# Performance work log

Measured on AMD Instinct MI355X. Metric: run time of the kernel, lower is better.

Reference implementation:

```python
import jax, jax.numpy as jnp
import numpy as np

EMBED_DIM = 2048
NUM_HEADS = 16
HEAD_DIM = EMBED_DIM // NUM_HEADS
LATENT_DIM = 512


def setup_inputs() -> dict:
    key = jax.random.key(0)
    ks = jax.random.split(key, 6)
    s = 1.0 / np.sqrt(EMBED_DIM)
    sl = 1.0 / np.sqrt(LATENT_DIM)
    x = jax.random.normal(ks[0], (2, 2048, EMBED_DIM), dtype=jnp.float32)
    # nn.Linear stores weight as [out, in]; we keep [in, out] for x @ W
    W_q = jax.random.uniform(ks[1], (EMBED_DIM, EMBED_DIM), jnp.float32, -s, s)
    W_c = jax.random.uniform(ks[2], (EMBED_DIM, LATENT_DIM), jnp.float32, -s, s)
    W_k = jax.random.uniform(ks[3], (LATENT_DIM, EMBED_DIM), jnp.float32, -sl, sl)
    W_v = jax.random.uniform(ks[4], (LATENT_DIM, EMBED_DIM), jnp.float32, -sl, sl)
    W_o = jax.random.uniform(ks[5], (EMBED_DIM, EMBED_DIM), jnp.float32, -s, s)
    return {"x": x, "W_q": W_q, "W_c": W_c, "W_k": W_k, "W_v": W_v, "W_o": W_o}


def reference(x, W_q, W_c, W_k, W_v, W_o):
    B, S, _ = x.shape
    H, D = NUM_HEADS, HEAD_DIM
    Q = (x @ W_q).reshape(B, S, H, D)          # [B,S,H,D]
    C = x @ W_c                                 # [B,S,latent]
    K = (C @ W_k).reshape(B, S, H, D)
    V = (C @ W_v).reshape(B, S, H, D)
    scale = 1.0 / np.sqrt(D).astype(np.float32)
    scores = jnp.einsum('bqhd,bkhd->bhqk', Q, K) * scale
    probs = jax.nn.softmax(scores, axis=-1)
    attn = jnp.einsum('bhqk,bkhd->bqhd', probs, V).reshape(B, S, H * D)
    return attn @ W_o
```

## Files before the change

### kernel.cpp

```cpp
#include <hip/hip_runtime.h>
#include <hip/hip_bf16.h>
#include <cstdint>
#include <cstddef>

#define EDIM 2048
#define SLEN 2048
#define BATCH 2
#define NH 16
#define HD 128
#define LAT 512
#define MROWS (BATCH * SLEN)

#define QPREMUL (0.08838834764831845f * 1.44269504088896340f)

typedef __bf16 bf16;
typedef __bf16 bf16x8 __attribute__((ext_vector_type(8)));
typedef __bf16 bf16x4 __attribute__((ext_vector_type(4)));
typedef float f32x4 __attribute__((ext_vector_type(4)));
typedef float f32x16 __attribute__((ext_vector_type(16)));

#define AS1 __attribute__((address_space(1)))
#define AS3 __attribute__((address_space(3)))

__device__ __forceinline__ void gload_lds16(const void* g, void* l) {
  __builtin_amdgcn_global_load_lds((const AS1 void*)g, (AS3 void*)l, 16, 0, 0);
}

__global__ __launch_bounds__(256) void cvt_f32_bf16(const float* __restrict__ in,
                                                    bf16* __restrict__ out, int n4) {
  int i = blockIdx.x * blockDim.x + threadIdx.x;
  int stride = gridDim.x * blockDim.x;
  for (; i < n4; i += stride) {
    float4 v = reinterpret_cast<const float4*>(in)[i];
    bf16x4 o = {(bf16)v.x, (bf16)v.y, (bf16)v.z, (bf16)v.w};
    reinterpret_cast<bf16x4*>(out)[i] = o;
  }
}

__global__ __launch_bounds__(256) void transpose_cvt(const float* __restrict__ W,
                                                     bf16* __restrict__ Wt,
                                                     int K, int N) {
  __shared__ float tile[32][33];
  const int tx = threadIdx.x, ty = threadIdx.y;
  const int n0 = blockIdx.x * 32, k0 = blockIdx.y * 32;
#pragma unroll
  for (int i = 0; i < 4; ++i)
    tile[ty + i * 8][tx] = W[(size_t)(k0 + ty + i * 8) * N + n0 + tx];
  __syncthreads();
#pragma unroll
  for (int i = 0; i < 4; ++i)
    Wt[(size_t)(n0 + ty + i * 8) * K + k0 + tx] = (bf16)tile[tx][ty + i * 8];
}

enum { P_F32 = 0, P_QC = 1, P_FRAGKV = 2 };

#define BUFSZ 24576

#define STAGE_B_UNIT(dstbuf, k0)                                                 \
  {                                                                              \
    _Pragma("unroll") for (int jj = 0; jj < 2; ++jj) {                           \
      int L = t + jj * 512;                                                      \
      int row = L >> 3, c = L & 7;                                               \
      gload_lds16(Bt + (size_t)(n0 + row) * K + (k0) + ((c ^ (row & 7)) << 3),   \
                  (dstbuf) + 16384 + L * 8);                                     \
    }                                                                            \
  }

#define STAGE_A_PART(dstbuf, k0, jj)                                             \
  {                                                                              \
    int L = t256 + (jj) * 256;                                                   \
    int row = ahalf * 128 + (L >> 3), c = L & 7;                                 \
    gload_lds16(A + (size_t)(m0 + row) * K + (k0) + ((c ^ (row & 7)) << 3),      \
                (dstbuf) + row * 64 + c * 8);                                    \
  }

template <int MODE>
__global__ __launch_bounds__(512, 1)
void gemm8p(const bf16* __restrict__ A, const bf16* __restrict__ Bt,
            float* __restrict__ Cf, bf16* __restrict__ Cb, bf16* __restrict__ Cb2,
            int M, int N, int K) {
  extern __shared__ bf16 lds[];
  const int t = threadIdx.x;
  const int wid = t >> 6, l = t & 63, lo = l & 15, hi = l >> 4;
  const int wr = wid >> 1, wc = wid & 1;
  const int lin = blockIdx.y * gridDim.x + blockIdx.x;
  const int cpx = (gridDim.x * gridDim.y) >> 3;
  const int sw = (lin & 7) * cpx + (lin >> 3);
  const int m0 = (sw / gridDim.x) * 256, n0 = (sw % gridDim.x) * 128;
  const int nk = K >> 6;
  const int t256 = t & 255, ahalf = t >> 8;

  int aoff[2][4], boff[2][4];
#pragma unroll
  for (int kk = 0; kk < 2; ++kk)
#pragma unroll
    for (int m = 0; m < 4; ++m) {
      int ra = wr * 64 + m * 16 + lo;
      aoff[kk][m] = ra * 64 + (((kk * 4 + hi) ^ (ra & 7)) << 3);
      int rb = wc * 64 + m * 16 + lo;
      boff[kk][m] = 16384 + rb * 64 + (((kk * 4 + hi) ^ (rb & 7)) << 3);
    }

  f32x4 acc[4][4] = {};

  {
    bf16* b0 = lds;
    STAGE_B_UNIT(b0, 0);
    STAGE_A_PART(b0, 0, 0); STAGE_A_PART(b0, 0, 1);
    STAGE_A_PART(b0, 0, 2); STAGE_A_PART(b0, 0, 3);
    if (nk > 1) {
      bf16* b1 = lds + BUFSZ;
      STAGE_B_UNIT(b1, 64);
      STAGE_A_PART(b1, 64, 0); STAGE_A_PART(b1, 64, 1);
      STAGE_A_PART(b1, 64, 2); STAGE_A_PART(b1, 64, 3);
      asm volatile("s_waitcnt vmcnt(6)" ::: "memory");
    } else {
      asm volatile("s_waitcnt vmcnt(0)" ::: "memory");
    }
    __builtin_amdgcn_s_barrier();
  }

  int bsel = 0;
  for (int tt = 0; tt < nk; ++tt) {
    bf16* buf = lds + bsel * BUFSZ;
    bf16* nb = lds + ((bsel + 2) % 3) * BUFSZ;
    const bool pre = (tt + 2) < nk;
    const int k2 = (tt + 2) << 6;
    bf16x8 af[4], bfr[4];

#pragma unroll
    for (int m = 0; m < 4; ++m) af[m] = *reinterpret_cast<const bf16x8*>(buf + aoff[0][m]);
#pragma unroll
    for (int n = 0; n < 4; ++n) bfr[n] = *reinterpret_cast<const bf16x8*>(buf + boff[0][n]);
    if (pre) {
      STAGE_B_UNIT(nb, k2);
      STAGE_A_PART(nb, k2, 0); STAGE_A_PART(nb, k2, 1);
    }
    __builtin_amdgcn_s_barrier();
    asm volatile("s_waitcnt lgkmcnt(0)" ::: "memory");
    __builtin_amdgcn_s_setprio(1);
#pragma unroll
    for (int m = 0; m < 4; ++m)
#pragma unroll
      for (int n = 0; n < 4; ++n)
        acc[m][n] = __builtin_amdgcn_mfma_f32_16x16x32_bf16(af[m], bfr[n], acc[m][n], 0, 0, 0);
    __builtin_amdgcn_s_setprio(0);
    __builtin_amdgcn_s_barrier();

#pragma unroll
    for (int m = 0; m < 4; ++m) af[m] = *reinterpret_cast<const bf16x8*>(buf + aoff[1][m]);
#pragma unroll
    for (int n = 0; n < 4; ++n) bfr[n] = *reinterpret_cast<const bf16x8*>(buf + boff[1][n]);
    if (pre) { STAGE_A_PART(nb, k2, 2); STAGE_A_PART(nb, k2, 3); }
    __builtin_amdgcn_s_barrier();
    asm volatile("s_waitcnt lgkmcnt(0)" ::: "memory");
    __builtin_amdgcn_s_setprio(1);
#pragma unroll
    for (int m = 0; m < 4; ++m)
#pragma unroll
      for (int n = 0; n < 4; ++n)
        acc[m][n] = __builtin_amdgcn_mfma_f32_16x16x32_bf16(af[m], bfr[n], acc[m][n], 0, 0, 0);
    __builtin_amdgcn_s_setprio(0);
    if (tt < nk - 2) {
      asm volatile("s_waitcnt vmcnt(6)" ::: "memory");
    } else if (tt == nk - 2) {
      asm volatile("s_waitcnt vmcnt(0)" ::: "memory");
    }
    __builtin_amdgcn_s_barrier();
    bsel = (bsel == 2) ? 0 : bsel + 1;
  }

  const int bb = m0 >> 11, m0r = m0 & 2047;

  if constexpr (MODE == P_F32) {
#pragma unroll
    for (int m = 0; m < 4; ++m) {
      const int rowb = m0 + wr * 64 + m * 16 + hi * 4;
#pragma unroll
      for (int n = 0; n < 4; ++n) {
        const int col = n0 + wc * 64 + n * 16 + lo;
        f32x4 v = acc[m][n];
#pragma unroll
        for (int r = 0; r < 4; ++r) Cf[(size_t)(rowb + r) * N + col] = v[r];
      }
    }
  } else if (MODE == P_QC && n0 >= EDIM) {
#pragma unroll
    for (int m = 0; m < 4; ++m) {
      const int rowb = m0 + wr * 64 + m * 16 + hi * 4;
#pragma unroll
      for (int n = 0; n < 4; ++n) {
        const int col = n0 + wc * 64 + n * 16 + lo;
        f32x4 v = acc[m][n];
#pragma unroll
        for (int r = 0; r < 4; ++r)
          Cb2[(size_t)(rowb + r) * LAT + (col - EDIM)] = (bf16)v[r];
      }
    }
  } else if (MODE == P_FRAGKV && n0 >= EDIM) {
    __syncthreads();
#pragma unroll
    for (int m = 0; m < 4; ++m) {
      const int row0 = wr * 64 + m * 16 + hi * 4;
#pragma unroll
      for (int n = 0; n < 4; ++n) {
        const int colr = wc * 64 + n * 16 + lo;
        f32x4 v = acc[m][n];
        bf16x4 pk = {(bf16)v[0], (bf16)v[1], (bf16)v[2], (bf16)v[3]};
        *reinterpret_cast<bf16x4*>(lds + colr * 264 + row0) = pk;
      }
    }
    __syncthreads();
    const int hv = (n0 - EDIM) >> 7;
#pragma unroll
    for (int k2i = 0; k2i < 8; ++k2i) {
      int c = t + k2i * 512;
      int qs64 = c >> 10, d7b = (c >> 8) & 3, sb = (c >> 5) & 7, d7l = c & 31;
      int col = d7b * 32 + d7l, row = qs64 * 64 + sb * 8;
      bf16x8 val = *reinterpret_cast<const bf16x8*>(lds + col * 264 + row);
      size_t addr = (((size_t)(bb * NH + hv) * 32 + (m0r >> 6) + qs64) << 14) + 8192 +
                    d7b * 2048 + sb * 256 + d7l * 8;
      *reinterpret_cast<bf16x8*>(Cb + addr) = val;
    }
  } else {
    constexpr bool ISQ = (MODE == P_QC);
    __syncthreads();
#pragma unroll
    for (int m = 0; m < 4; ++m) {
      const int row0 = wr * 64 + m * 16 + hi * 4;
#pragma unroll
      for (int n = 0; n < 4; ++n) {
        const int colr = wc * 64 + n * 16 + lo;
        f32x4 v = acc[m][n];
#pragma unroll
        for (int r = 0; r < 4; ++r)
          lds[(row0 + r) * 132 + colr] = ISQ ? (bf16)(v[r] * QPREMUL) : (bf16)v[r];
      }
    }
    __syncthreads();
    const int hh = n0 >> 7;
#pragma unroll
    for (int k2i = 0; k2i < 8; ++k2i) {
      int c = t + k2i * 512;
      int qsub = c >> 9, frag = (c >> 5) & 15, lane = c & 31;
      int row = qsub * 32 + lane;
      bf16x4 lo4 = *reinterpret_cast<const bf16x4*>(lds + row * 132 + frag * 8);
      bf16x4 hi4 = *reinterpret_cast<const bf16x4*>(lds + row * 132 + frag * 8 + 4);
      size_t addr;
      if constexpr (ISQ)
        addr = (((size_t)(bb * NH + hh) * 64 + (m0r >> 5) + qsub) << 12) +
               frag * 256 + lane * 8;
      else
        addr = (((size_t)(bb * NH + hh) * 32 + (m0r >> 6) + (qsub >> 1)) << 14) +
               ((qsub & 1) << 12) + frag * 256 + lane * 8;
      union { bf16x4 h4[2]; bf16x8 v8; } u;
      u.h4[0] = lo4; u.h4[1] = hi4;
      *reinterpret_cast<bf16x8*>(Cb + addr) = u.v8;
    }
  }
}

#define ATT_STAGE(st_)                                                            \
  {                                                                               \
    const int T_ = (st_) >> 1, hh_ = (st_) & 1;                                   \
    bf16* d_ = sbuf[(st_) & 3];                                                   \
    const bf16* s_ = KV + T_ * 16384;                                             \
    int c_ = t;                                                                   \
    gload_lds16(s_ + hh_ * 4096 + c_ * 8, d_ + c_ * 8);                           \
    int db_ = c_ >> 7, cw_ = c_ & 127;                                            \
    gload_lds16(s_ + 8192 + db_ * 2048 + hh_ * 1024 + cw_ * 8,                    \
                d_ + 4096 + c_ * 8);                                              \
  }

#define ATT_QK(st_, sb_)                                                          \
  {                                                                               \
    const bf16* sk_ = (sb_);                                                      \
    st_ = f32x16{};                                                               \
    __builtin_amdgcn_s_setprio(1);                                                \
    _Pragma("unroll") for (int ks = 0; ks < 8; ++ks) {                            \
      bf16x8 kf = *reinterpret_cast<const bf16x8*>(sk_ + ks * 512 + l * 8);       \
      st_ = __builtin_amdgcn_mfma_f32_32x32x16_bf16(kf, qf[ks], st_, 0, 0, 0);    \
    }                                                                             \
    __builtin_amdgcn_s_setprio(0);                                                \
  }

#define ATT_SMPACK(st_, pa_)                                                      \
  {                                                                               \
    float ts_ = 0.f;                                                              \
    _Pragma("unroll") for (int r = 0; r < 16; ++r) {                              \
      float e_ = __builtin_amdgcn_exp2f(st_[r]);                                  \
      st_[r] = e_;                                                                \
      ts_ += e_;                                                                  \
    }                                                                             \
    lsum += ts_;                                                                  \
    _Pragma("unroll") for (int fh = 0; fh < 2; ++fh) {                            \
      union W2 { bf16 h2[2]; unsigned u; };                                       \
      W2 a_, b_, c_, d2_;                                                         \
      a_.h2[0] = (bf16)st_[8 * fh + 0]; a_.h2[1] = (bf16)st_[8 * fh + 1];         \
      b_.h2[0] = (bf16)st_[8 * fh + 4]; b_.h2[1] = (bf16)st_[8 * fh + 5];         \
      c_.h2[0] = (bf16)st_[8 * fh + 2]; c_.h2[1] = (bf16)st_[8 * fh + 3];         \
      d2_.h2[0] = (bf16)st_[8 * fh + 6]; d2_.h2[1] = (bf16)st_[8 * fh + 7];       \
      unsigned sAB = hi1 ? a_.u : b_.u;                                           \
      unsigned gAB = __shfl_xor(sAB, 32);                                         \
      unsigned w0 = hi1 ? gAB : a_.u;                                             \
      unsigned w2 = hi1 ? b_.u : gAB;                                             \
      unsigned sCD = hi1 ? c_.u : d2_.u;                                          \
      unsigned gCD = __shfl_xor(sCD, 32);                                         \
      unsigned w1 = hi1 ? gCD : c_.u;                                             \
      unsigned w3 = hi1 ? d2_.u : gCD;                                            \
      union FW { unsigned wd[4]; bf16x8 v; } fw;                                  \
      fw.wd[0] = w0; fw.wd[1] = w1; fw.wd[2] = w2; fw.wd[3] = w3;                 \
      pa_[fh] = fw.v;                                                             \
    }                                                                             \
  }

#define ATT_PV(pa_, sb_)                                                          \
  {                                                                               \
    const bf16* sv_ = (sb_) + 4096;                                               \
    __builtin_amdgcn_s_setprio(1);                                                \
    _Pragma("unroll") for (int db = 0; db < 4; ++db)                              \
      _Pragma("unroll") for (int ksl = 0; ksl < 2; ++ksl) {                       \
        bf16x8 vf = *reinterpret_cast<const bf16x8*>(sv_ + db * 1024 +            \
                                                     ksl * 512 + l * 8);          \
        ot[db] = __builtin_amdgcn_mfma_f32_32x32x16_bf16(vf, pa_[ksl], ot[db],    \
                                                         0, 0, 0);                \
      }                                                                           \
    __builtin_amdgcn_s_setprio(0);                                                \
  }

__global__ __launch_bounds__(512) void attn_fwd32(const bf16* __restrict__ Qf,
                                                  const bf16* __restrict__ KVf,
                                                  bf16* __restrict__ O) {
  __shared__ bf16 sbuf[4][8192];
  const int t = threadIdx.x, w = t >> 6, l = t & 63;
  const int q = l & 31, hi1 = l >> 5;
  const int wg = blockIdx.y * 8 + blockIdx.x;
  const int wgs = (wg & 7) * 16 + (wg >> 3);
  const int qt = wgs & 7, h = wgs >> 3;
  const int b = blockIdx.z;
  const int bh = b * NH + h;
  const bf16* KV = KVf + (size_t)bh * (32 * 16384);
  const size_t qbase = ((size_t)bh * 64 + qt * 8 + w) * 4096;

  bf16x8 qf[8];
#pragma unroll
  for (int ks = 0; ks < 8; ++ks)
    qf[ks] = *reinterpret_cast<const bf16x8*>(Qf + qbase + ks * 512 + l * 8);
  asm volatile("s_waitcnt vmcnt(0)" ::: "memory");

  f32x16 ot[4] = {};
  float lsum = 0.f;
  f32x16 stA, stB;
  bf16x8 paA[2], paB[2];

  ATT_STAGE(0);
  ATT_STAGE(1);
  asm volatile("s_waitcnt vmcnt(2)" ::: "memory");
  __builtin_amdgcn_s_barrier();
  ATT_QK(stA, sbuf[0]);
  ATT_STAGE(2);

  for (int tt = 1; tt < 63; tt += 2) {
    asm volatile("s_waitcnt vmcnt(2)" ::: "memory");
    __builtin_amdgcn_s_barrier();
    ATT_QK(stB, sbuf[tt & 3]);
    ATT_SMPACK(stA, paA);
    ATT_STAGE(tt + 2);
    ATT_PV(paA, sbuf[(tt - 1) & 3]);
    asm volatile("s_waitcnt vmcnt(2)" ::: "memory");
    __builtin_amdgcn_s_barrier();
    ATT_QK(stA, sbuf[(tt + 1) & 3]);
    ATT_SMPACK(stB, paB);
    if (tt + 3 < 64) ATT_STAGE(tt + 3);
    ATT_PV(paB, sbuf[tt & 3]);
  }

  asm volatile("s_waitcnt vmcnt(0)" ::: "memory");
  __builtin_amdgcn_s_barrier();
  ATT_QK(stB, sbuf[3]);
  ATT_SMPACK(stA, paA);
  ATT_PV(paA, sbuf[2]);
  ATT_SMPACK(stB, paB);
  ATT_PV(paB, sbuf[3]);

  const float linv = 1.0f / (lsum + __shfl_xor(lsum, 32));
  const size_t orow = ((size_t)b * SLEN + qt * 256 + w * 32 + q) * EDIM + h * HD;
#pragma unroll
  for (int db = 0; db < 4; ++db)
#pragma unroll
    for (int g = 0; g < 4; ++g) {
      bf16x4 ov = {(bf16)(ot[db][4 * g + 0] * linv), (bf16)(ot[db][4 * g + 1] * linv),
                   (bf16)(ot[db][4 * g + 2] * linv), (bf16)(ot[db][4 * g + 3] * linv)};
      *reinterpret_cast<bf16x4*>(&O[orow + db * 32 + 8 * g + 4 * hi1]) = ov;
    }
}

extern "C" void kernel_launch(void* const* d_in, const int* in_sizes, int n_in,
                              void* d_out, int out_size, void* d_ws, size_t ws_size,
                              hipStream_t stream) {
  const float* x  = (const float*)d_in[0];
  const float* Wq = (const float*)d_in[1];
  const float* Wc = (const float*)d_in[2];
  const float* Wk = (const float*)d_in[3];
  const float* Wv = (const float*)d_in[4];
  const float* Wo = (const float*)d_in[5];
  float* out = (float*)d_out;

  char* ws = (char*)d_ws;
  size_t off = 0;
  auto alloc = [&](size_t bytes) {
    void* p = ws + off;
    off += (bytes + 255) & ~(size_t)255;
    return p;
  };
  bf16* XB   = (bf16*)alloc((size_t)MROWS * EDIM * 2);
  bf16* WQCT = (bf16*)alloc((size_t)(EDIM + LAT) * EDIM * 2);
  bf16* WKVT = (bf16*)alloc((size_t)2 * EDIM * LAT * 2);
  bf16* WOT  = (bf16*)alloc((size_t)EDIM * EDIM * 2);
  bf16* Qfr  = (bf16*)alloc((size_t)MROWS * EDIM * 2);
  bf16* Cm   = (bf16*)alloc((size_t)MROWS * LAT * 2);
  bf16* KVf  = (bf16*)alloc((size_t)2 * MROWS * EDIM * 2);
  bf16* Am   = (bf16*)alloc((size_t)MROWS * EDIM * 2);
  (void)ws_size; (void)in_sizes; (void)n_in; (void)out_size;

  const int LDSB = BUFSZ * 3 * 2;
  hipFuncSetAttribute((const void*)&gemm8p<P_QC>,     hipFuncAttributeMaxDynamicSharedMemorySize, LDSB);
  hipFuncSetAttribute((const void*)&gemm8p<P_FRAGKV>, hipFuncAttributeMaxDynamicSharedMemorySize, LDSB);
  hipFuncSetAttribute((const void*)&gemm8p<P_F32>,    hipFuncAttributeMaxDynamicSharedMemorySize, LDSB);

  dim3 tb(32, 8);
  cvt_f32_bf16<<<4096, 256, 0, stream>>>(x, XB, MROWS * EDIM / 4);
  transpose_cvt<<<dim3(EDIM / 32, EDIM / 32), tb, 0, stream>>>(Wq, WQCT, EDIM, EDIM);
  transpose_cvt<<<dim3(LAT / 32, EDIM / 32), tb, 0, stream>>>(Wc, WQCT + (size_t)EDIM * EDIM, EDIM, LAT);
  transpose_cvt<<<dim3(EDIM / 32, LAT / 32), tb, 0, stream>>>(Wk, WKVT, LAT, EDIM);
  transpose_cvt<<<dim3(EDIM / 32, LAT / 32), tb, 0, stream>>>(Wv, WKVT + (size_t)EDIM * LAT, LAT, EDIM);
  transpose_cvt<<<dim3(EDIM / 32, EDIM / 32), tb, 0, stream>>>(Wo, WOT, EDIM, EDIM);

  gemm8p<P_QC><<<dim3((EDIM + LAT) / 128, MROWS / 256), 512, LDSB, stream>>>(
      XB, WQCT, nullptr, Qfr, Cm, MROWS, EDIM + LAT, EDIM);
  gemm8p<P_FRAGKV><<<dim3(2 * EDIM / 128, MROWS / 256), 512, LDSB, stream>>>(
      Cm, WKVT, nullptr, KVf, nullptr, MROWS, 2 * EDIM, LAT);

  attn_fwd32<<<dim3(SLEN / 256, NH, BATCH), 512, 0, stream>>>(Qfr, KVf, Am);

  gemm8p<P_F32><<<dim3(EDIM / 128, MROWS / 256), 512, LDSB, stream>>>(
      Am, WOT, out, nullptr, nullptr, MROWS, EDIM, EDIM);
}
```

Before: 233.4 us.

## Split attention KV range across two wave groups and merge partial outputs in LDS

The attention kernel now uses 128 query rows per workgroup instead of 256, with 4 query groups times 2 KV halves. The two halves process disjoint key ranges and their partial outputs and row sums are combined through LDS at the end. This doubles the grid to raise parallelism and cut per-block sequential work. In exchange it drops the software-pipelined QK/softmax/PV overlap for a simpler loop that fully waits on loads each step, adds a reduction pass, and uses more LDS. The merge assumes both halves share the same softmax max (fixed-offset exp), which holds only if SMPACK does not track a running max.

```diff
diff --git a/kernel.cpp b/kernel.cpp
--- a/kernel.cpp
+++ b/kernel.cpp
@@ -260,16 +260,15 @@
   }
 }
 
-#define ATT_STAGE(st_)                                                            \
+#define ATT_STAGE2(Tabs_, dst_)                                                   \
   {                                                                               \
-    const int T_ = (st_) >> 1, hh_ = (st_) & 1;                                   \
-    bf16* d_ = sbuf[(st_) & 3];                                                   \
+    const int T_ = (Tabs_) >> 1, hh_ = (Tabs_) & 1;                               \
     const bf16* s_ = KV + T_ * 16384;                                             \
     int c_ = t;                                                                   \
-    gload_lds16(s_ + hh_ * 4096 + c_ * 8, d_ + c_ * 8);                           \
+    gload_lds16(s_ + hh_ * 4096 + c_ * 8, (dst_) + c_ * 8);                       \
     int db_ = c_ >> 7, cw_ = c_ & 127;                                            \
     gload_lds16(s_ + 8192 + db_ * 2048 + hh_ * 1024 + cw_ * 8,                    \
-                d_ + 4096 + c_ * 8);                                              \
+                (dst_) + 4096 + c_ * 8);                                          \
   }
 
 #define ATT_QK(st_, sb_)                                                          \
@@ -331,16 +330,18 @@
 __global__ __launch_bounds__(512) void attn_fwd32(const bf16* __restrict__ Qf,
                                                   const bf16* __restrict__ KVf,
                                                   bf16* __restrict__ O) {
-  __shared__ bf16 sbuf[4][8192];
+  extern __shared__ __align__(16) char smem[];
+  bf16* sbase = (bf16*)smem;
   const int t = threadIdx.x, w = t >> 6, l = t & 63;
   const int q = l & 31, hi1 = l >> 5;
-  const int wg = blockIdx.y * 8 + blockIdx.x;
-  const int wgs = (wg & 7) * 16 + (wg >> 3);
-  const int qt = wgs & 7, h = wgs >> 3;
+  const int qg = w & 3, kh = w >> 2;
+  const int wg = blockIdx.y * 16 + blockIdx.x;
+  const int wgs = (wg & 7) * 32 + (wg >> 3);
+  const int qt = wgs & 15, h = wgs >> 4;
   const int b = blockIdx.z;
   const int bh = b * NH + h;
   const bf16* KV = KVf + (size_t)bh * (32 * 16384);
-  const size_t qbase = ((size_t)bh * 64 + qt * 8 + w) * 4096;
+  const size_t qbase = ((size_t)bh * 64 + qt * 4 + qg) * 4096;
 
   bf16x8 qf[8];
 #pragma unroll
@@ -350,49 +351,60 @@
 
   f32x16 ot[4] = {};
   float lsum = 0.f;
-  f32x16 stA, stB;
-  bf16x8 paA[2], paB[2];
-
-  ATT_STAGE(0);
-  ATT_STAGE(1);
-  asm volatile("s_waitcnt vmcnt(2)" ::: "memory");
-  __builtin_amdgcn_s_barrier();
-  ATT_QK(stA, sbuf[0]);
-  ATT_STAGE(2);
-
-  for (int tt = 1; tt < 63; tt += 2) {
-    asm volatile("s_waitcnt vmcnt(2)" ::: "memory");
-    __builtin_amdgcn_s_barrier();
-    ATT_QK(stB, sbuf[tt & 3]);
-    ATT_SMPACK(stA, paA);
-    ATT_STAGE(tt + 2);
-    ATT_PV(paA, sbuf[(tt - 1) & 3]);
-    asm volatile("s_waitcnt vmcnt(2)" ::: "memory");
-    __builtin_amdgcn_s_barrier();
-    ATT_QK(stA, sbuf[(tt + 1) & 3]);
-    ATT_SMPACK(stB, paB);
-    if (tt + 3 < 64) ATT_STAGE(tt + 3);
-    ATT_PV(paB, sbuf[tt & 3]);
-  }
-
-  asm volatile("s_waitcnt vmcnt(0)" ::: "memory");
-  __builtin_amdgcn_s_barrier();
-  ATT_QK(stB, sbuf[3]);
-  ATT_SMPACK(stA, paA);
-  ATT_PV(paA, sbuf[2]);
-  ATT_SMPACK(stB, paB);
-  ATT_PV(paB, sbuf[3]);
-
-  const float linv = 1.0f / (lsum + __shfl_xor(lsum, 32));
-  const size_t orow = ((size_t)b * SLEN + qt * 256 + w * 32 + q) * EDIM + h * HD;
-#pragma unroll
-  for (int db = 0; db < 4; ++db)
-#pragma unroll
-    for (int g = 0; g < 4; ++g) {
-      bf16x4 ov = {(bf16)(ot[db][4 * g + 0] * linv), (bf16)(ot[db][4 * g + 1] * linv),
-                   (bf16)(ot[db][4 * g + 2] * linv), (bf16)(ot[db][4 * g + 3] * linv)};
-      *reinterpret_cast<bf16x4*>(&O[orow + db * 32 + 8 * g + 4 * hi1]) = ov;
-    }
+  f32x16 st;
+  bf16x8 pa[2];
+
+  ATT_STAGE2(0, sbase);
+  ATT_STAGE2(32, sbase + 2 * 8192);
+
+  for (int tt = 0; tt < 32; ++tt) {
+    asm volatile("s_waitcnt vmcnt(0)" ::: "memory");
+    __builtin_amdgcn_s_barrier();
+    if (tt + 1 < 32) {
+      ATT_STAGE2(tt + 1, sbase + ((tt + 1) & 1) * 8192);
+      ATT_STAGE2(33 + tt, sbase + (2 + ((tt + 1) & 1)) * 8192);
+    }
+    const bf16* sb = sbase + (kh * 2 + (tt & 1)) * 8192;
+    ATT_QK(st, sb);
+    ATT_SMPACK(st, pa);
+    ATT_PV(pa, sb);
+  }
+
+  __syncthreads();
+  float* base = (float*)smem + qg * 4416;
+  if (kh == 1) {
+#pragma unroll
+    for (int db = 0; db < 4; ++db)
+#pragma unroll
+      for (int rr = 0; rr < 4; ++rr) {
+        f32x4 v = {ot[db][4 * rr + 0], ot[db][4 * rr + 1],
+                   ot[db][4 * rr + 2], ot[db][4 * rr + 3]};
+        *reinterpret_cast<f32x4*>(base + l * 68 + db * 16 + rr * 4) = v;
+      }
+    base[4352 + l] = lsum;
+  }
+  __syncthreads();
+  if (kh == 0) {
+#pragma unroll
+    for (int db = 0; db < 4; ++db)
+#pragma unroll
+      for (int rr = 0; rr < 4; ++rr) {
+        f32x4 v = *reinterpret_cast<const f32x4*>(base + l * 68 + db * 16 + rr * 4);
+        ot[db][4 * rr + 0] += v[0]; ot[db][4 * rr + 1] += v[1];
+        ot[db][4 * rr + 2] += v[2]; ot[db][4 * rr + 3] += v[3];
+      }
+    lsum += base[4352 + l];
+    const float linv = 1.0f / (lsum + __shfl_xor(lsum, 32));
+    const size_t orow = ((size_t)b * SLEN + qt * 128 + qg * 32 + q) * EDIM + h * HD;
+#pragma unroll
+    for (int db = 0; db < 4; ++db)
+#pragma unroll
+      for (int g = 0; g < 4; ++g) {
+        bf16x4 ov = {(bf16)(ot[db][4 * g + 0] * linv), (bf16)(ot[db][4 * g + 1] * linv),
+                     (bf16)(ot[db][4 * g + 2] * linv), (bf16)(ot[db][4 * g + 3] * linv)};
+        *reinterpret_cast<bf16x4*>(&O[orow + db * 32 + 8 * g + 4 * hi1]) = ov;
+      }
+  }
 }
 
 extern "C" void kernel_launch(void* const* d_in, const int* in_sizes, int n_in,
@@ -424,9 +436,11 @@
   (void)ws_size; (void)in_sizes; (void)n_in; (void)out_size;
 
   const int LDSB = BUFSZ * 3 * 2;
+  const int ALDS = 70912;
   hipFuncSetAttribute((const void*)&gemm8p<P_QC>,     hipFuncAttributeMaxDynamicSharedMemorySize, LDSB);
   hipFuncSetAttribute((const void*)&gemm8p<P_FRAGKV>, hipFuncAttributeMaxDynamicSharedMemorySize, LDSB);
   hipFuncSetAttribute((const void*)&gemm8p<P_F32>,    hipFuncAttributeMaxDynamicSharedMemorySize, LDSB);
+  hipFuncSetAttribute((const void*)&attn_fwd32,       hipFuncAttributeMaxDynamicSharedMemorySize, ALDS);
 
   dim3 tb(32, 8);
   cvt_f32_bf16<<<4096, 256, 0, stream>>>(x, XB, MROWS * EDIM / 4);
@@ -441,7 +455,7 @@
   gemm8p<P_FRAGKV><<<dim3(2 * EDIM / 128, MROWS / 256), 512, LDSB, stream>>>(
       Cm, WKVT, nullptr, KVf, nullptr, MROWS, 2 * EDIM, LAT);
 
-  attn_fwd32<<<dim3(SLEN / 256, NH, BATCH), 512, 0, stream>>>(Qfr, KVf, Am);
+  attn_fwd32<<<dim3(16, 16, BATCH), 512, ALDS, stream>>>(Qfr, KVf, Am);
 
   gemm8p<P_F32><<<dim3(EDIM / 128, MROWS / 256), 512, LDSB, stream>>>(
       Am, WOT, out, nullptr, nullptr, MROWS, EDIM, EDIM);
```

Measured after the change: 239.8 us. 2.7% more time.
